# Kernel tuning notes

Measured on AMD Instinct MI355X. Metric: run time of the kernel, lower is better.

Reference implementation:

```python
import jax, jax.numpy as jnp
import numpy as np

NUM = 4
EPS = 1e-8


def setup_inputs() -> dict:
    key = jax.random.key(0)
    ks = jax.random.split(key, 8)
    B, N, D = 64, 1024, 512
    x = jax.random.normal(ks[0], (B, N, D), dtype=jnp.float32)
    # marginal priors: valid probability distributions (log is taken inside)
    p0 = jax.nn.softmax(jax.random.normal(ks[1], (B, 1, D), dtype=jnp.float32), axis=2)
    q0 = jax.nn.softmax(jax.random.normal(ks[2], (B, N, 1), dtype=jnp.float32), axis=1)
    # strictly positive regularization weights / ADMM step sizes
    a1 = jax.random.uniform(ks[3], (NUM,), dtype=jnp.float32, minval=0.1, maxval=1.1)
    a2 = jax.random.uniform(ks[4], (NUM,), dtype=jnp.float32, minval=0.1, maxval=1.1)
    a3 = jax.random.uniform(ks[5], (NUM,), dtype=jnp.float32, minval=0.1, maxval=1.1)
    rho = jax.random.uniform(ks[6], (NUM,), dtype=jnp.float32, minval=0.1, maxval=1.1)
    mask = jnp.ones((B, N, 1), dtype=jnp.float32)
    return {"x": x, "p0": p0, "q0": q0, "a1": a1, "a2": a2, "a3": a3,
            "rho": rho, "mask": mask}


def _lse(y, axis):
    return jax.scipy.special.logsumexp(y, axis=axis, keepdims=True)


def _masked_log_colsum(y, mask):
    # stable log(sum_n exp(y)*mask) over axis 1, masking as in the torch code
    ymin = jnp.min(y, axis=1, keepdims=True)
    ymax = jnp.max(ymin - mask * ymin + y, axis=1, keepdims=True)
    lse = jnp.log(jnp.sum(jnp.exp((y - ymax) * mask) * mask, axis=1, keepdims=True))
    return lse, ymax


def uot_badmm(x, p0, q0, a1, a2, a3, rho, mask, num=NUM, eps=EPS):
    log_p0 = jnp.log(p0)                      # (B,1,D)
    log_q0 = jnp.log(q0 + eps) * mask         # (B,N,1)
    log_t = (log_q0 + log_p0) * mask          # (B,N,D)
    log_s = (log_q0 + log_p0) * mask
    log_mu = jnp.log(p0)
    log_eta = jnp.log(q0 + eps) * mask
    z = jnp.zeros_like(log_t)
    z1 = jnp.zeros_like(p0)
    z2 = jnp.zeros_like(q0)
    for k in range(num):
        n = min(k, a1.shape[0] - 1)
        rn = rho[n]
        # t-update
        y = (x - z) / rn + log_s
        log_t = mask * (log_eta - _lse(y, 2)) + y
        # s-update
        y = (z + rn * log_t) / (a1[n] + rn)
        lse, ymax = _masked_log_colsum(y, mask)
        log_s = mask * (log_mu - lse - ymax) + y
        t = jnp.exp(log_t) * mask
        s = jnp.exp(log_s) * mask
        z = z + rn * (t - s)
        # mu-update
        y = (rn * log_mu + a2[n] * log_p0 - z1) / (rn + a2[n])
        log_mu = y - _lse(y, 2)
        # eta-update
        y = (rn * log_eta + a3[n] * log_q0 - z2) / (rn + a3[n])
        lse, ymax = _masked_log_colsum(y, mask)
        log_eta = (y - lse - ymax) * mask
        # dual updates
        z1 = z1 + rn * (jnp.exp(log_mu) - jnp.sum(s, axis=1, keepdims=True))
        z2 = z2 + rn * (jnp.exp(log_eta) * mask - jnp.sum(t, axis=2, keepdims=True)) * mask
    return jnp.exp(log_t) * mask


def reference(x, p0, q0, a1, a2, a3, rho, mask):
    return uot_badmm(x, p0, q0, a1, a2, a3, rho, mask, num=NUM, eps=EPS)
```

## Files before the change

### kernel.cpp

```cpp
#include <hip/hip_runtime.h>
#include <math.h>

#define BB 64
#define NN 1024
#define DD 512
#define SEG 64
#define ROWS_PER_BLOCK 16
#define ROWS_PER_WAVE 4
#define WAVES 4
#define EPSQ 1e-8f
#define L2E 1.44269504088896340736f

typedef _Float16 h8 __attribute__((ext_vector_type(8)));
typedef float f32x4 __attribute__((ext_vector_type(4)));

#if __has_builtin(__builtin_amdgcn_exp2f)
__device__ __forceinline__ float ex2(float x) { return __builtin_amdgcn_exp2f(x); }
#else
__device__ __forceinline__ float ex2(float x) { return exp2f(x); }
#endif
#if __has_builtin(__builtin_amdgcn_logf)
__device__ __forceinline__ float lg2(float x) { return __builtin_amdgcn_logf(x); }
#else
__device__ __forceinline__ float lg2(float x) { return log2f(x); }
#endif

__device__ __forceinline__ float wmax(float v) {
#pragma unroll
    for (int o = 32; o; o >>= 1) v = fmaxf(v, __shfl_xor(v, o));
    return v;
}
__device__ __forceinline__ float wsum(float v) {
#pragma unroll
    for (int o = 32; o; o >>= 1) v += __shfl_xor(v, o);
    return v;
}
template <int NW>
__device__ __forceinline__ float block_max(float v, float* lds) {
    v = wmax(v);
    __syncthreads();
    if ((threadIdx.x & 63) == 0) lds[threadIdx.x >> 6] = v;
    __syncthreads();
    float r = lds[0];
#pragma unroll
    for (int i = 1; i < NW; i++) r = fmaxf(r, lds[i]);
    return r;
}
template <int NW>
__device__ __forceinline__ float block_sum(float v, float* lds) {
    v = wsum(v);
    __syncthreads();
    if ((threadIdx.x & 63) == 0) lds[threadIdx.x >> 6] = v;
    __syncthreads();
    float r = 0.f;
#pragma unroll
    for (int i = 0; i < NW; i++) r += lds[i];
    return r;
}

__device__ __forceinline__ void load8(float* r, const float* p) {
    float4 a = *reinterpret_cast<const float4*>(p);
    float4 b = *reinterpret_cast<const float4*>(p + 4);
    r[0] = a.x; r[1] = a.y; r[2] = a.z; r[3] = a.w;
    r[4] = b.x; r[5] = b.y; r[6] = b.z; r[7] = b.w;
}
__device__ __forceinline__ void load8_nt(float* r, const float* p) {
    f32x4 a = __builtin_nontemporal_load(reinterpret_cast<const f32x4*>(p));
    f32x4 b = __builtin_nontemporal_load(reinterpret_cast<const f32x4*>(p) + 1);
    r[0] = a.x; r[1] = a.y; r[2] = a.z; r[3] = a.w;
    r[4] = b.x; r[5] = b.y; r[6] = b.z; r[7] = b.w;
}
__device__ __forceinline__ void store8_nt(float* p, const float* r) {
    f32x4 a, b;
    a.x = r[0]; a.y = r[1]; a.z = r[2]; a.w = r[3];
    b.x = r[4]; b.y = r[5]; b.z = r[6]; b.w = r[7];
    __builtin_nontemporal_store(a, reinterpret_cast<f32x4*>(p));
    __builtin_nontemporal_store(b, reinterpret_cast<f32x4*>(p) + 1);
}

__global__ __launch_bounds__(512) void small_seq_kernel(
    const float* __restrict__ p0, const float* __restrict__ q0,
    const float* __restrict__ a2, const float* __restrict__ a3,
    const float* __restrict__ rho, float* __restrict__ lmu_seq,
    float* __restrict__ leta_seq, float* __restrict__ lp_tab) {
    __shared__ float lds[8];
    const int b = blockIdx.x, t = threadIdx.x;
    const float lp = lg2(p0[b * DD + t]);
    lp_tab[b * DD + t] = lp;
    const float lqa = lg2(q0[b * NN + t] + EPSQ);
    const float lqb = lg2(q0[b * NN + t + 512] + EPSQ);
    float lmu = lp, lea = lqa, leb = lqb;
    float z1 = 0.f, z2a = 0.f, z2b = 0.f;
    lmu_seq[b * DD + t] = lmu;
    leta_seq[b * NN + t] = lea;
    leta_seq[b * NN + t + 512] = leb;
    for (int k = 0; k < 4; k++) {
        const float r = rho[k], A2 = a2[k], A3 = a3[k];
        const float rL = r * L2E;
        float y = (r * lmu + A2 * lp - z1) / (r + A2);
        float m = block_max<8>(y, lds);
        float S = block_sum<8>(ex2(y - m), lds);
        float lse = m + lg2(S);
        float lmun = y - lse;
        z1 += rL * (ex2(lmun) - ex2(lmu));
        lmu = lmun;
        if (k < 2) lmu_seq[(size_t)(k + 1) * (BB * DD) + b * DD + t] = lmu;
        float ya = (r * lea + A3 * lqa - z2a) / (r + A3);
        float yb = (r * leb + A3 * lqb - z2b) / (r + A3);
        m = block_max<8>(fmaxf(ya, yb), lds);
        S = block_sum<8>(ex2(ya - m) + ex2(yb - m), lds);
        lse = m + lg2(S);
        float lean = ya - lse, lebn = yb - lse;
        z2a += rL * (ex2(lean) - ex2(lea));
        z2b += rL * (ex2(lebn) - ex2(leb));
        lea = lean;
        leb = lebn;
        if (k < 3) {
            leta_seq[(size_t)(k + 1) * (BB * NN) + b * NN + t] = lea;
            leta_seq[(size_t)(k + 1) * (BB * NN) + b * NN + t + 512] = leb;
        }
    }
}

__global__ __launch_bounds__(256, 4) void a0_kernel(
    const float* __restrict__ x, const float* __restrict__ lp_tab,
    const float* __restrict__ leta_seq, _Float16* __restrict__ x16,
    float* __restrict__ crow, float* __restrict__ psum,
    const float* __restrict__ a1, const float* __restrict__ rho) {
    __shared__ float sms[WAVES][DD];
    const int b = blockIdx.x >> 6, seg = blockIdx.x & 63;
    const int w = threadIdx.x >> 6, l = threadIdx.x & 63;
    const int d0 = l * 8;
    const float r0 = rho[0];
    const float inv_r0 = 1.f / r0;
    const float inv_ar0 = 1.f / (a1[0] + r0);

    float lp[8];
    load8(lp, lp_tab + b * DD + d0);
    const float* lrowq = leta_seq + b * NN;

    float ss[8];
#pragma unroll
    for (int j = 0; j < 8; j++) ss[j] = 0.f;

    const int row0 = seg * ROWS_PER_BLOCK + w * ROWS_PER_WAVE;
#pragma unroll 2
    for (int i = 0; i < ROWS_PER_WAVE; i++) {
        const int n = row0 + i;
        const size_t base = ((size_t)b * NN + n) * DD + d0;
        const float lq = lrowq[n];
        float xv[8];
        load8_nt(xv, x + base);
        h8 xh;
#pragma unroll
        for (int j = 0; j < 8; j++) xh[j] = (_Float16)(xv[j] * L2E);
        *reinterpret_cast<h8*>(x16 + base) = xh;
        float yb[8];
        float ml = -INFINITY;
#pragma unroll
        for (int j = 0; j < 8; j++) {
            float xs = (float)xh[j];
            yb[j] = fmaf(xs, inv_r0, lq + lp[j]);
            ml = fmaxf(ml, yb[j]);
        }
        float m = wmax(ml);
        float se = 0.f;
#pragma unroll
        for (int j = 0; j < 8; j++) se += ex2(yb[j] - m);
        float lse = m + lg2(wsum(se));
        const float c = lq - lse;
        if (l == 0) crow[b * NN + n] = c;
#pragma unroll
        for (int j = 0; j < 8; j++) {
            float lt = c + yb[j];
            ss[j] += ex2((r0 * lt) * inv_ar0);
        }
    }
#pragma unroll
    for (int j = 0; j < 8; j += 4)
        *reinterpret_cast<float4*>(&sms[w][d0 + j]) =
            make_float4(ss[j], ss[j + 1], ss[j + 2], ss[j + 3]);
    __syncthreads();
    for (int d = threadIdx.x; d < DD; d += 256) {
        float S = sms[0][d] + sms[1][d] + sms[2][d] + sms[3][d];
        psum[((size_t)b * SEG + seg) * DD + d] = S;
    }
}

__global__ __launch_bounds__(256) void colfin_kernel(
    const float* __restrict__ psum, const float* __restrict__ lmu_seq,
    float* __restrict__ cc_tab, int k) {
    const int idx = blockIdx.x * 256 + threadIdx.x;
    const int b = idx >> 9, d = idx & (DD - 1);
    float S = 0.f;
    for (int s = 0; s < SEG; s++)
        S += psum[((size_t)b * SEG + s) * DD + d];
    cc_tab[(size_t)k * (BB * DD) + idx] =
        lmu_seq[(size_t)k * (BB * DD) + idx] - lg2(S);
}

template <int K, bool LAST>
__global__ __launch_bounds__(256, 4) void f_kernel(
    const _Float16* __restrict__ x16, float* __restrict__ out,
    const float* __restrict__ lp_tab, const float* __restrict__ leta_seq,
    float* __restrict__ crow, const float* __restrict__ cc_tab,
    float* __restrict__ psum, const float* __restrict__ a1,
    const float* __restrict__ rho) {
    __shared__ float sms[WAVES][DD];
    const int b = blockIdx.x >> 6, seg = blockIdx.x & 63;
    const int w = threadIdx.x >> 6, l = threadIdx.x & 63;
    const int d0 = l * 8;

    float rv[K + 1], invr[K + 1], rLv[K + 1], invar[K + 1];
#pragma unroll
    for (int i = 0; i <= K; i++) {
        rv[i] = rho[i];
        invr[i] = 1.f / rv[i];
        rLv[i] = rv[i] * L2E;
        invar[i] = 1.f / (a1[i] + rv[i]);
    }

    float lp[8];
    load8(lp, lp_tab + b * DD + d0);
    float ccv[K][8];
#pragma unroll
    for (int i = 0; i < K; i++)
        load8(ccv[i], cc_tab + (size_t)i * (BB * DD) + b * DD + d0);

    const float* lrowq = leta_seq + b * NN;
    const float* lrowK = leta_seq + (size_t)K * (BB * NN) + b * NN;

    float ss[8];
#pragma unroll
    for (int j = 0; j < 8; j++) ss[j] = 0.f;

    const int row0 = seg * ROWS_PER_BLOCK + w * ROWS_PER_WAVE;
#pragma unroll 2
    for (int i0 = 0; i0 < ROWS_PER_WAVE; i0++) {
        const int n = row0 + i0;
        const size_t base = ((size_t)b * NN + n) * DD + d0;
        h8 xh;
        if (LAST)
            xh = __builtin_nontemporal_load(
                reinterpret_cast<const h8*>(x16 + base));
        else
            xh = *reinterpret_cast<const h8*>(x16 + base);
        const float lq = lrowq[n];
        float cr[K];
#pragma unroll
        for (int i = 0; i < K; i++) cr[i] = crow[(size_t)i * (BB * NN) + b * NN + n];
        const float letaK = lrowK[n];
        float yb[8], znj[8];
        float ml = -INFINITY;
#pragma unroll
        for (int j = 0; j < 8; j++) {
            float xs = (float)xh[j];
            float y = fmaf(xs, invr[0], lq + lp[j]);
            float lt = cr[0] + y;
            float zn = 0.f;
#pragma unroll
            for (int i = 1; i <= K; i++) {
                float y2v = (zn + rv[i - 1] * lt) * invar[i - 1];
                float ls = ccv[i - 1][j] + y2v;
                zn = zn + rLv[i - 1] * (ex2(lt) - ex2(ls));
                y = fmaf(xs - zn, invr[i], ls);
                if (i < K) lt = cr[i] + y;
            }
            yb[j] = y;
            znj[j] = zn;
            ml = fmaxf(ml, y);
        }
        float m = wmax(ml);
        float se = 0.f;
#pragma unroll
        for (int j = 0; j < 8; j++) se += ex2(yb[j] - m);
        float lse = m + lg2(wsum(se));
        const float c = letaK - lse;
        if (LAST) {
            float o[8];
#pragma unroll
            for (int j = 0; j < 8; j++) o[j] = ex2(c + yb[j]);
            store8_nt(out + base, o);
        } else {
            if (l == 0) crow[(size_t)K * (BB * NN) + b * NN + n] = c;
#pragma unroll
            for (int j = 0; j < 8; j++) {
                float lt = c + yb[j];
                float y2K = (znj[j] + rv[K] * lt) * invar[K];
                ss[j] += ex2(y2K);
            }
        }
    }
    if (!LAST) {
#pragma unroll
        for (int j = 0; j < 8; j += 4)
            *reinterpret_cast<float4*>(&sms[w][d0 + j]) =
                make_float4(ss[j], ss[j + 1], ss[j + 2], ss[j + 3]);
        __syncthreads();
        for (int d = threadIdx.x; d < DD; d += 256) {
            float S = sms[0][d] + sms[1][d] + sms[2][d] + sms[3][d];
            psum[((size_t)b * SEG + seg) * DD + d] = S;
        }
    }
}

extern "C" void kernel_launch(void* const* d_in, const int* in_sizes, int n_in,
                              void* d_out, int out_size, void* d_ws,
                              size_t ws_size, hipStream_t stream) {
    (void)in_sizes; (void)n_in; (void)out_size; (void)ws_size;
    const float* x = (const float*)d_in[0];
    const float* p0 = (const float*)d_in[1];
    const float* q0 = (const float*)d_in[2];
    const float* a1 = (const float*)d_in[3];
    const float* a2 = (const float*)d_in[4];
    const float* a3 = (const float*)d_in[5];
    const float* rho = (const float*)d_in[6];
    float* out = (float*)d_out;

    char* w = (char*)d_ws;
    _Float16* x16 = (_Float16*)w;  w += (size_t)BB * NN * DD * 2;
    float* lmu_seq = (float*)w;    w += (size_t)3 * BB * DD * 4;
    float* leta_seq = (float*)w;   w += (size_t)4 * BB * NN * 4;
    float* psum = (float*)w;       w += (size_t)BB * SEG * DD * 4;
    float* cc_tab = (float*)w;     w += (size_t)3 * BB * DD * 4;
    float* crow = (float*)w;       w += (size_t)3 * BB * NN * 4;
    float* lp_tab = (float*)w;

    const int blocks = BB * SEG;
    const int cfin_blocks = (BB * DD) / 256;

    small_seq_kernel<<<BB, 512, 0, stream>>>(p0, q0, a2, a3, rho, lmu_seq,
                                             leta_seq, lp_tab);
    a0_kernel<<<blocks, 256, 0, stream>>>(x, lp_tab, leta_seq, x16, crow, psum,
                                          a1, rho);

    colfin_kernel<<<cfin_blocks, 256, 0, stream>>>(psum, lmu_seq, cc_tab, 0);
    f_kernel<1, false><<<blocks, 256, 0, stream>>>(
        x16, out, lp_tab, leta_seq, crow, cc_tab, psum, a1, rho);

    colfin_kernel<<<cfin_blocks, 256, 0, stream>>>(psum, lmu_seq, cc_tab, 1);
    f_kernel<2, false><<<blocks, 256, 0, stream>>>(
        x16, out, lp_tab, leta_seq, crow, cc_tab, psum, a1, rho);

    colfin_kernel<<<cfin_blocks, 256, 0, stream>>>(psum, lmu_seq, cc_tab, 2);
    f_kernel<3, true><<<blocks, 256, 0, stream>>>(
        x16, out, lp_tab, leta_seq, crow, cc_tab, psum, a1, rho);
}
```

Measured before the change: 185.8 us.

## Fuse marginal sequence and column finalize into streaming kernels, halve segment count

Folds the small mu/eta sequence kernel into the first streaming kernel, which seg-0 blocks compute, and moves the column-sum finalize into the start of each f_kernel. Every block now redundantly reduces the partial sums into LDS. It also doubles rows per block, halving the number of segments, and recomputes log p0/q0 on the fly instead of reading tables. This cuts four launches and their serialization gaps, at the cost of redundant per-block reductions and a longer seg-0 block.

Result: slower. 190.8 us (+2.7%).

```diff
diff --git a/kernel.cpp b/kernel.cpp
--- a/kernel.cpp
+++ b/kernel.cpp
@@ -4,10 +4,11 @@
 #define BB 64
 #define NN 1024
 #define DD 512
-#define SEG 64
-#define ROWS_PER_BLOCK 16
-#define ROWS_PER_WAVE 4
+#define SEG 32
+#define ROWS_PER_BLOCK 32
+#define ROWS_PER_WAVE 8
 #define WAVES 4
+#define NBLK (BB * SEG)
 #define EPSQ 1e-8f
 #define L2E 1.44269504088896340736f
 
@@ -78,67 +79,85 @@
     __builtin_nontemporal_store(b, reinterpret_cast<f32x4*>(p) + 1);
 }
 
-__global__ __launch_bounds__(512) void small_seq_kernel(
-    const float* __restrict__ p0, const float* __restrict__ q0,
+__global__ __launch_bounds__(256, 4) void k1_kernel(
+    const float* __restrict__ x, const float* __restrict__ p0,
+    const float* __restrict__ q0, const float* __restrict__ a1,
     const float* __restrict__ a2, const float* __restrict__ a3,
-    const float* __restrict__ rho, float* __restrict__ lmu_seq,
-    float* __restrict__ leta_seq, float* __restrict__ lp_tab) {
-    __shared__ float lds[8];
-    const int b = blockIdx.x, t = threadIdx.x;
-    const float lp = lg2(p0[b * DD + t]);
-    lp_tab[b * DD + t] = lp;
-    const float lqa = lg2(q0[b * NN + t] + EPSQ);
-    const float lqb = lg2(q0[b * NN + t + 512] + EPSQ);
-    float lmu = lp, lea = lqa, leb = lqb;
-    float z1 = 0.f, z2a = 0.f, z2b = 0.f;
-    lmu_seq[b * DD + t] = lmu;
-    leta_seq[b * NN + t] = lea;
-    leta_seq[b * NN + t + 512] = leb;
-    for (int k = 0; k < 4; k++) {
-        const float r = rho[k], A2 = a2[k], A3 = a3[k];
-        const float rL = r * L2E;
-        float y = (r * lmu + A2 * lp - z1) / (r + A2);
-        float m = block_max<8>(y, lds);
-        float S = block_sum<8>(ex2(y - m), lds);
-        float lse = m + lg2(S);
-        float lmun = y - lse;
-        z1 += rL * (ex2(lmun) - ex2(lmu));
-        lmu = lmun;
-        if (k < 2) lmu_seq[(size_t)(k + 1) * (BB * DD) + b * DD + t] = lmu;
-        float ya = (r * lea + A3 * lqa - z2a) / (r + A3);
-        float yb = (r * leb + A3 * lqb - z2b) / (r + A3);
-        m = block_max<8>(fmaxf(ya, yb), lds);
-        S = block_sum<8>(ex2(ya - m) + ex2(yb - m), lds);
-        lse = m + lg2(S);
-        float lean = ya - lse, lebn = yb - lse;
-        z2a += rL * (ex2(lean) - ex2(lea));
-        z2b += rL * (ex2(lebn) - ex2(leb));
-        lea = lean;
-        leb = lebn;
-        if (k < 3) {
-            leta_seq[(size_t)(k + 1) * (BB * NN) + b * NN + t] = lea;
-            leta_seq[(size_t)(k + 1) * (BB * NN) + b * NN + t + 512] = leb;
-        }
-    }
-}
-
-__global__ __launch_bounds__(256, 4) void a0_kernel(
-    const float* __restrict__ x, const float* __restrict__ lp_tab,
-    const float* __restrict__ leta_seq, _Float16* __restrict__ x16,
-    float* __restrict__ crow, float* __restrict__ psum,
-    const float* __restrict__ a1, const float* __restrict__ rho) {
+    const float* __restrict__ rho, _Float16* __restrict__ x16,
+    float* __restrict__ lmu_seq, float* __restrict__ leta_seq,
+    float* __restrict__ crow, float* __restrict__ psumA) {
     __shared__ float sms[WAVES][DD];
-    const int b = blockIdx.x >> 6, seg = blockIdx.x & 63;
-    const int w = threadIdx.x >> 6, l = threadIdx.x & 63;
+    __shared__ float s_red[8];
+    const int tid = threadIdx.x;
+    const int b = blockIdx.x >> 5, seg = blockIdx.x & 31;
+    const int w = tid >> 6, l = tid & 63;
     const int d0 = l * 8;
+
+    if (seg == 0) {
+        const float lpA = lg2(p0[b * DD + tid]);
+        const float lpB = lg2(p0[b * DD + tid + 256]);
+        float lqv[4], lev[4], z2v[4];
+#pragma unroll
+        for (int u = 0; u < 4; u++) {
+            lqv[u] = lg2(q0[b * NN + tid + 256 * u] + EPSQ);
+            lev[u] = lqv[u];
+            z2v[u] = 0.f;
+            leta_seq[b * NN + tid + 256 * u] = lqv[u];
+        }
+        float lmuA = lpA, lmuB = lpB, z1A = 0.f, z1B = 0.f;
+        lmu_seq[b * DD + tid] = lmuA;
+        lmu_seq[b * DD + tid + 256] = lmuB;
+        for (int k = 0; k < 3; k++) {
+            const float r = rho[k], A2 = a2[k], A3 = a3[k];
+            const float rL = r * L2E;
+            float yA = (r * lmuA + A2 * lpA - z1A) / (r + A2);
+            float yB = (r * lmuB + A2 * lpB - z1B) / (r + A2);
+            float m = block_max<4>(fmaxf(yA, yB), s_red);
+            float S = block_sum<4>(ex2(yA - m) + ex2(yB - m), s_red);
+            float lse = m + lg2(S);
+            float lmuAn = yA - lse, lmuBn = yB - lse;
+            z1A += rL * (ex2(lmuAn) - ex2(lmuA));
+            z1B += rL * (ex2(lmuBn) - ex2(lmuB));
+            lmuA = lmuAn;
+            lmuB = lmuBn;
+            if (k < 2) {
+                lmu_seq[(size_t)(k + 1) * (BB * DD) + b * DD + tid] = lmuA;
+                lmu_seq[(size_t)(k + 1) * (BB * DD) + b * DD + tid + 256] = lmuB;
+            }
+            float yv[4];
+            float ml = -INFINITY;
+#pragma unroll
+            for (int u = 0; u < 4; u++) {
+                yv[u] = (r * lev[u] + A3 * lqv[u] - z2v[u]) / (r + A3);
+                ml = fmaxf(ml, yv[u]);
+            }
+            m = block_max<4>(ml, s_red);
+            float se = 0.f;
+#pragma unroll
+            for (int u = 0; u < 4; u++) se += ex2(yv[u] - m);
+            S = block_sum<4>(se, s_red);
+            lse = m + lg2(S);
+#pragma unroll
+            for (int u = 0; u < 4; u++) {
+                float ln = yv[u] - lse;
+                z2v[u] += rL * (ex2(ln) - ex2(lev[u]));
+                lev[u] = ln;
+                leta_seq[(size_t)(k + 1) * (BB * NN) + b * NN + tid + 256 * u] = ln;
+            }
+        }
+        __syncthreads();
+    }
+
     const float r0 = rho[0];
     const float inv_r0 = 1.f / r0;
     const float inv_ar0 = 1.f / (a1[0] + r0);
-
     float lp[8];
-    load8(lp, lp_tab + b * DD + d0);
-    const float* lrowq = leta_seq + b * NN;
-
+    {
+        float tmp[8];
+        load8(tmp, p0 + b * DD + d0);
+#pragma unroll
+        for (int j = 0; j < 8; j++) lp[j] = lg2(tmp[j]);
+    }
     float ss[8];
 #pragma unroll
     for (int j = 0; j < 8; j++) ss[j] = 0.f;
@@ -148,7 +167,7 @@
     for (int i = 0; i < ROWS_PER_WAVE; i++) {
         const int n = row0 + i;
         const size_t base = ((size_t)b * NN + n) * DD + d0;
-        const float lq = lrowq[n];
+        const float lq = lg2(q0[b * NN + n] + EPSQ);
         float xv[8];
         load8_nt(xv, x + base);
         h8 xh;
@@ -171,64 +190,70 @@
         const float c = lq - lse;
         if (l == 0) crow[b * NN + n] = c;
 #pragma unroll
-        for (int j = 0; j < 8; j++) {
-            float lt = c + yb[j];
-            ss[j] += ex2((r0 * lt) * inv_ar0);
-        }
+        for (int j = 0; j < 8; j++) ss[j] += ex2((r0 * (c + yb[j])) * inv_ar0);
     }
 #pragma unroll
     for (int j = 0; j < 8; j += 4)
         *reinterpret_cast<float4*>(&sms[w][d0 + j]) =
             make_float4(ss[j], ss[j + 1], ss[j + 2], ss[j + 3]);
     __syncthreads();
-    for (int d = threadIdx.x; d < DD; d += 256) {
+    for (int d = tid; d < DD; d += 256) {
         float S = sms[0][d] + sms[1][d] + sms[2][d] + sms[3][d];
-        psum[((size_t)b * SEG + seg) * DD + d] = S;
-    }
-}
-
-__global__ __launch_bounds__(256) void colfin_kernel(
-    const float* __restrict__ psum, const float* __restrict__ lmu_seq,
-    float* __restrict__ cc_tab, int k) {
-    const int idx = blockIdx.x * 256 + threadIdx.x;
-    const int b = idx >> 9, d = idx & (DD - 1);
-    float S = 0.f;
-    for (int s = 0; s < SEG; s++)
-        S += psum[((size_t)b * SEG + s) * DD + d];
-    cc_tab[(size_t)k * (BB * DD) + idx] =
-        lmu_seq[(size_t)k * (BB * DD) + idx] - lg2(S);
-}
-
-template <int K, bool LAST>
+        psumA[(size_t)blockIdx.x * DD + d] = S;
+    }
+}
+
+template <int P, bool LAST>
 __global__ __launch_bounds__(256, 4) void f_kernel(
     const _Float16* __restrict__ x16, float* __restrict__ out,
-    const float* __restrict__ lp_tab, const float* __restrict__ leta_seq,
-    float* __restrict__ crow, const float* __restrict__ cc_tab,
-    float* __restrict__ psum, const float* __restrict__ a1,
+    const float* __restrict__ p0, const float* __restrict__ lmu_seq,
+    const float* __restrict__ leta_seq, float* __restrict__ crow,
+    float* __restrict__ cc_tab, const float* __restrict__ psum_in,
+    float* __restrict__ psum_out, const float* __restrict__ a1,
     const float* __restrict__ rho) {
+    __shared__ float s_cc[P][DD];
     __shared__ float sms[WAVES][DD];
-    const int b = blockIdx.x >> 6, seg = blockIdx.x & 63;
-    const int w = threadIdx.x >> 6, l = threadIdx.x & 63;
+    const int tid = threadIdx.x;
+    const int b = blockIdx.x >> 5, seg = blockIdx.x & 31;
+    const int w = tid >> 6, l = tid & 63;
     const int d0 = l * 8;
 
-    float rv[K + 1], invr[K + 1], rLv[K + 1], invar[K + 1];
-#pragma unroll
-    for (int i = 0; i <= K; i++) {
+    float rv[P + 1], invr[P + 1], rLv[P + 1], invar[P + 1];
+#pragma unroll
+    for (int i = 0; i <= P; i++) {
         rv[i] = rho[i];
         invr[i] = 1.f / rv[i];
         rLv[i] = rv[i] * L2E;
         invar[i] = 1.f / (a1[i] + rv[i]);
     }
 
+    for (int d = tid; d < DD; d += 256) {
+#pragma unroll
+        for (int i = 0; i + 1 < P; i++)
+            s_cc[i][d] = cc_tab[(size_t)i * (BB * DD) + b * DD + d];
+        float S = 0.f;
+        for (int s = 0; s < SEG; s++)
+            S += psum_in[((size_t)(b * SEG + s)) * DD + d];
+        float ccP = lmu_seq[(size_t)(P - 1) * (BB * DD) + b * DD + d] - lg2(S);
+        s_cc[P - 1][d] = ccP;
+        if (!LAST && seg == 0)
+            cc_tab[(size_t)(P - 1) * (BB * DD) + b * DD + d] = ccP;
+    }
+    __syncthreads();
+
     float lp[8];
-    load8(lp, lp_tab + b * DD + d0);
-    float ccv[K][8];
-#pragma unroll
-    for (int i = 0; i < K; i++)
-        load8(ccv[i], cc_tab + (size_t)i * (BB * DD) + b * DD + d0);
-
-    const float* lrowq = leta_seq + b * NN;
-    const float* lrowK = leta_seq + (size_t)K * (BB * NN) + b * NN;
+    {
+        float tmp[8];
+        load8(tmp, p0 + b * DD + d0);
+#pragma unroll
+        for (int j = 0; j < 8; j++) lp[j] = lg2(tmp[j]);
+    }
+    float ccv[P][8];
+#pragma unroll
+    for (int i = 0; i < P; i++) load8(ccv[i], &s_cc[i][d0]);
+
+    const float* lrow0 = leta_seq + b * NN;
+    const float* lrowP = leta_seq + (size_t)P * (BB * NN) + b * NN;
 
     float ss[8];
 #pragma unroll
@@ -245,50 +270,47 @@
                 reinterpret_cast<const h8*>(x16 + base));
         else
             xh = *reinterpret_cast<const h8*>(x16 + base);
-        const float lq = lrowq[n];
-        float cr[K];
-#pragma unroll
-        for (int i = 0; i < K; i++) cr[i] = crow[(size_t)i * (BB * NN) + b * NN + n];
-        const float letaK = lrowK[n];
-        float yb[8], znj[8];
+        const float lq = lrow0[n];
+        float cr[P];
+#pragma unroll
+        for (int i = 0; i < P; i++)
+            cr[i] = crow[(size_t)i * (BB * NN) + b * NN + n];
+        float y[8], z[8];
         float ml = -INFINITY;
 #pragma unroll
         for (int j = 0; j < 8; j++) {
             float xs = (float)xh[j];
-            float y = fmaf(xs, invr[0], lq + lp[j]);
-            float lt = cr[0] + y;
-            float zn = 0.f;
-#pragma unroll
-            for (int i = 1; i <= K; i++) {
-                float y2v = (zn + rv[i - 1] * lt) * invar[i - 1];
-                float ls = ccv[i - 1][j] + y2v;
-                zn = zn + rLv[i - 1] * (ex2(lt) - ex2(ls));
-                y = fmaf(xs - zn, invr[i], ls);
-                if (i < K) lt = cr[i] + y;
+            float yy = fmaf(xs, invr[0], lq + lp[j]);
+            float lt = cr[0] + yy;
+            float zz = 0.f;
+#pragma unroll
+            for (int i2 = 1; i2 <= P; i2++) {
+                float y2v = (zz + rv[i2 - 1] * lt) * invar[i2 - 1];
+                float ls = ccv[i2 - 1][j] + y2v;
+                zz += rLv[i2 - 1] * (ex2(lt) - ex2(ls));
+                yy = fmaf(xs - zz, invr[i2], ls);
+                if (i2 < P) lt = cr[i2] + yy;
             }
-            yb[j] = y;
-            znj[j] = zn;
-            ml = fmaxf(ml, y);
+            y[j] = yy;
+            z[j] = zz;
+            ml = fmaxf(ml, yy);
         }
         float m = wmax(ml);
         float se = 0.f;
 #pragma unroll
-        for (int j = 0; j < 8; j++) se += ex2(yb[j] - m);
+        for (int j = 0; j < 8; j++) se += ex2(y[j] - m);
         float lse = m + lg2(wsum(se));
-        const float c = letaK - lse;
+        const float c = lrowP[n] - lse;
         if (LAST) {
             float o[8];
 #pragma unroll
-            for (int j = 0; j < 8; j++) o[j] = ex2(c + yb[j]);
+            for (int j = 0; j < 8; j++) o[j] = ex2(c + y[j]);
             store8_nt(out + base, o);
         } else {
-            if (l == 0) crow[(size_t)K * (BB * NN) + b * NN + n] = c;
-#pragma unroll
-            for (int j = 0; j < 8; j++) {
-                float lt = c + yb[j];
-                float y2K = (znj[j] + rv[K] * lt) * invar[K];
-                ss[j] += ex2(y2K);
-            }
+            if (l == 0) crow[(size_t)P * (BB * NN) + b * NN + n] = c;
+#pragma unroll
+            for (int j = 0; j < 8; j++)
+                ss[j] += ex2((z[j] + rv[P] * (c + y[j])) * invar[P]);
         }
     }
     if (!LAST) {
@@ -297,9 +319,9 @@
             *reinterpret_cast<float4*>(&sms[w][d0 + j]) =
                 make_float4(ss[j], ss[j + 1], ss[j + 2], ss[j + 3]);
         __syncthreads();
-        for (int d = threadIdx.x; d < DD; d += 256) {
+        for (int d = tid; d < DD; d += 256) {
             float S = sms[0][d] + sms[1][d] + sms[2][d] + sms[3][d];
-            psum[((size_t)b * SEG + seg) * DD + d] = S;
+            psum_out[(size_t)blockIdx.x * DD + d] = S;
         }
     }
 }
@@ -321,28 +343,17 @@
     _Float16* x16 = (_Float16*)w;  w += (size_t)BB * NN * DD * 2;
     float* lmu_seq = (float*)w;    w += (size_t)3 * BB * DD * 4;
     float* leta_seq = (float*)w;   w += (size_t)4 * BB * NN * 4;
-    float* psum = (float*)w;       w += (size_t)BB * SEG * DD * 4;
-    float* cc_tab = (float*)w;     w += (size_t)3 * BB * DD * 4;
-    float* crow = (float*)w;       w += (size_t)3 * BB * NN * 4;
-    float* lp_tab = (float*)w;
-
-    const int blocks = BB * SEG;
-    const int cfin_blocks = (BB * DD) / 256;
-
-    small_seq_kernel<<<BB, 512, 0, stream>>>(p0, q0, a2, a3, rho, lmu_seq,
-                                             leta_seq, lp_tab);
-    a0_kernel<<<blocks, 256, 0, stream>>>(x, lp_tab, leta_seq, x16, crow, psum,
-                                          a1, rho);
-
-    colfin_kernel<<<cfin_blocks, 256, 0, stream>>>(psum, lmu_seq, cc_tab, 0);
-    f_kernel<1, false><<<blocks, 256, 0, stream>>>(
-        x16, out, lp_tab, leta_seq, crow, cc_tab, psum, a1, rho);
-
-    colfin_kernel<<<cfin_blocks, 256, 0, stream>>>(psum, lmu_seq, cc_tab, 1);
-    f_kernel<2, false><<<blocks, 256, 0, stream>>>(
-        x16, out, lp_tab, leta_seq, crow, cc_tab, psum, a1, rho);
-
-    colfin_kernel<<<cfin_blocks, 256, 0, stream>>>(psum, lmu_seq, cc_tab, 2);
-    f_kernel<3, true><<<blocks, 256, 0, stream>>>(
-        x16, out, lp_tab, leta_seq, crow, cc_tab, psum, a1, rho);
-}
+    float* psumA = (float*)w;      w += (size_t)NBLK * DD * 4;
+    float* psumB = (float*)w;      w += (size_t)NBLK * DD * 4;
+    float* cc_tab = (float*)w;     w += (size_t)2 * BB * DD * 4;
+    float* crow = (float*)w;
+
+    k1_kernel<<<NBLK, 256, 0, stream>>>(x, p0, q0, a1, a2, a3, rho, x16,
+                                        lmu_seq, leta_seq, crow, psumA);
+    f_kernel<1, false><<<NBLK, 256, 0, stream>>>(
+        x16, out, p0, lmu_seq, leta_seq, crow, cc_tab, psumA, psumB, a1, rho);
+    f_kernel<2, false><<<NBLK, 256, 0, stream>>>(
+        x16, out, p0, lmu_seq, leta_seq, crow, cc_tab, psumB, psumA, a1, rho);
+    f_kernel<3, true><<<NBLK, 256, 0, stream>>>(
+        x16, out, p0, lmu_seq, leta_seq, crow, cc_tab, psumA, psumB, a1, rho);
+}
```

## Switch to single-wave blocks with per-wave column partial sums

Applied to the files above, without the earlier changes.

Blocks shrink from four waves to one wave of 64 threads covering 4 rows, which removes the LDS reduction and __syncthreads in the main kernels. Each block writes its own column partial sums, so the colfin reduction now reads 256 segments instead of 64. log2 of p0 and q0 is recomputed inside the kernels instead of being read from a precomputed table. Launch bounds differ per template stage, and psum uses ping-pong buffers. The cost is four times more partial-sum traffic and a longer serial loop in colfin.

New measurement: 249.8 us. 34.5% more time.

```diff
diff --git a/kernel.cpp b/kernel.cpp
--- a/kernel.cpp
+++ b/kernel.cpp
@@ -4,10 +4,9 @@
 #define BB 64
 #define NN 1024
 #define DD 512
-#define SEG 64
-#define ROWS_PER_BLOCK 16
-#define ROWS_PER_WAVE 4
-#define WAVES 4
+#define RPW 4
+#define SEGB (NN / RPW)
+#define NBLK (BB * SEGB)
 #define EPSQ 1e-8f
 #define L2E 1.44269504088896340736f
 
@@ -77,16 +76,22 @@
     __builtin_nontemporal_store(a, reinterpret_cast<f32x4*>(p));
     __builtin_nontemporal_store(b, reinterpret_cast<f32x4*>(p) + 1);
 }
+__device__ __forceinline__ void store8(float* p, const float* r) {
+    float4 a, b;
+    a.x = r[0]; a.y = r[1]; a.z = r[2]; a.w = r[3];
+    b.x = r[4]; b.y = r[5]; b.z = r[6]; b.w = r[7];
+    *reinterpret_cast<float4*>(p) = a;
+    *reinterpret_cast<float4*>(p + 4) = b;
+}
 
 __global__ __launch_bounds__(512) void small_seq_kernel(
     const float* __restrict__ p0, const float* __restrict__ q0,
     const float* __restrict__ a2, const float* __restrict__ a3,
     const float* __restrict__ rho, float* __restrict__ lmu_seq,
-    float* __restrict__ leta_seq, float* __restrict__ lp_tab) {
+    float* __restrict__ leta_seq) {
     __shared__ float lds[8];
     const int b = blockIdx.x, t = threadIdx.x;
     const float lp = lg2(p0[b * DD + t]);
-    lp_tab[b * DD + t] = lp;
     const float lqa = lg2(q0[b * NN + t] + EPSQ);
     const float lqb = lg2(q0[b * NN + t + 512] + EPSQ);
     float lmu = lp, lea = lqa, leb = lqb;
@@ -94,7 +99,7 @@
     lmu_seq[b * DD + t] = lmu;
     leta_seq[b * NN + t] = lea;
     leta_seq[b * NN + t + 512] = leb;
-    for (int k = 0; k < 4; k++) {
+    for (int k = 0; k < 3; k++) {
         const float r = rho[k], A2 = a2[k], A3 = a3[k];
         const float rL = r * L2E;
         float y = (r * lmu + A2 * lp - z1) / (r + A2);
@@ -115,40 +120,41 @@
         z2b += rL * (ex2(lebn) - ex2(leb));
         lea = lean;
         leb = lebn;
-        if (k < 3) {
-            leta_seq[(size_t)(k + 1) * (BB * NN) + b * NN + t] = lea;
-            leta_seq[(size_t)(k + 1) * (BB * NN) + b * NN + t + 512] = leb;
-        }
-    }
-}
-
-__global__ __launch_bounds__(256, 4) void a0_kernel(
-    const float* __restrict__ x, const float* __restrict__ lp_tab,
-    const float* __restrict__ leta_seq, _Float16* __restrict__ x16,
-    float* __restrict__ crow, float* __restrict__ psum,
+        leta_seq[(size_t)(k + 1) * (BB * NN) + b * NN + t] = lea;
+        leta_seq[(size_t)(k + 1) * (BB * NN) + b * NN + t + 512] = leb;
+    }
+}
+
+__global__ __launch_bounds__(64, 8) void a0_kernel(
+    const float* __restrict__ x, const float* __restrict__ p0,
+    const float* __restrict__ q0, _Float16* __restrict__ x16,
+    float* __restrict__ crow, float* __restrict__ psumA,
     const float* __restrict__ a1, const float* __restrict__ rho) {
-    __shared__ float sms[WAVES][DD];
-    const int b = blockIdx.x >> 6, seg = blockIdx.x & 63;
-    const int w = threadIdx.x >> 6, l = threadIdx.x & 63;
+    const int blk = blockIdx.x;
+    const int b = blk >> 8, seg = blk & 255;
+    const int l = threadIdx.x;
     const int d0 = l * 8;
     const float r0 = rho[0];
     const float inv_r0 = 1.f / r0;
     const float inv_ar0 = 1.f / (a1[0] + r0);
 
     float lp[8];
-    load8(lp, lp_tab + b * DD + d0);
-    const float* lrowq = leta_seq + b * NN;
-
+    {
+        float tmp[8];
+        load8(tmp, p0 + b * DD + d0);
+#pragma unroll
+        for (int j = 0; j < 8; j++) lp[j] = lg2(tmp[j]);
+    }
     float ss[8];
 #pragma unroll
     for (int j = 0; j < 8; j++) ss[j] = 0.f;
 
-    const int row0 = seg * ROWS_PER_BLOCK + w * ROWS_PER_WAVE;
+    const int row0 = seg * RPW;
 #pragma unroll 2
-    for (int i = 0; i < ROWS_PER_WAVE; i++) {
+    for (int i = 0; i < RPW; i++) {
         const int n = row0 + i;
         const size_t base = ((size_t)b * NN + n) * DD + d0;
-        const float lq = lrowq[n];
+        const float lq = lg2(q0[b * NN + n] + EPSQ);
         float xv[8];
         load8_nt(xv, x + base);
         h8 xh;
@@ -171,20 +177,9 @@
         const float c = lq - lse;
         if (l == 0) crow[b * NN + n] = c;
 #pragma unroll
-        for (int j = 0; j < 8; j++) {
-            float lt = c + yb[j];
-            ss[j] += ex2((r0 * lt) * inv_ar0);
-        }
-    }
-#pragma unroll
-    for (int j = 0; j < 8; j += 4)
-        *reinterpret_cast<float4*>(&sms[w][d0 + j]) =
-            make_float4(ss[j], ss[j + 1], ss[j + 2], ss[j + 3]);
-    __syncthreads();
-    for (int d = threadIdx.x; d < DD; d += 256) {
-        float S = sms[0][d] + sms[1][d] + sms[2][d] + sms[3][d];
-        psum[((size_t)b * SEG + seg) * DD + d] = S;
-    }
+        for (int j = 0; j < 8; j++) ss[j] += ex2((r0 * (c + yb[j])) * inv_ar0);
+    }
+    store8(psumA + (size_t)blk * DD + d0, ss);
 }
 
 __global__ __launch_bounds__(256) void colfin_kernel(
@@ -193,27 +188,27 @@
     const int idx = blockIdx.x * 256 + threadIdx.x;
     const int b = idx >> 9, d = idx & (DD - 1);
     float S = 0.f;
-    for (int s = 0; s < SEG; s++)
-        S += psum[((size_t)b * SEG + s) * DD + d];
+    for (int s = 0; s < SEGB; s++)
+        S += psum[((size_t)(b * SEGB + s)) * DD + d];
     cc_tab[(size_t)k * (BB * DD) + idx] =
         lmu_seq[(size_t)k * (BB * DD) + idx] - lg2(S);
 }
 
-template <int K, bool LAST>
-__global__ __launch_bounds__(256, 4) void f_kernel(
+template <int P, bool LAST, int MINW>
+__global__ __launch_bounds__(64, MINW) void f_kernel(
     const _Float16* __restrict__ x16, float* __restrict__ out,
-    const float* __restrict__ lp_tab, const float* __restrict__ leta_seq,
+    const float* __restrict__ p0, const float* __restrict__ leta_seq,
     float* __restrict__ crow, const float* __restrict__ cc_tab,
-    float* __restrict__ psum, const float* __restrict__ a1,
+    float* __restrict__ psum_out, const float* __restrict__ a1,
     const float* __restrict__ rho) {
-    __shared__ float sms[WAVES][DD];
-    const int b = blockIdx.x >> 6, seg = blockIdx.x & 63;
-    const int w = threadIdx.x >> 6, l = threadIdx.x & 63;
+    const int blk = blockIdx.x;
+    const int b = blk >> 8, seg = blk & 255;
+    const int l = threadIdx.x;
     const int d0 = l * 8;
 
-    float rv[K + 1], invr[K + 1], rLv[K + 1], invar[K + 1];
-#pragma unroll
-    for (int i = 0; i <= K; i++) {
+    float rv[P + 1], invr[P + 1], rLv[P + 1], invar[P + 1];
+#pragma unroll
+    for (int i = 0; i <= P; i++) {
         rv[i] = rho[i];
         invr[i] = 1.f / rv[i];
         rLv[i] = rv[i] * L2E;
@@ -221,22 +216,27 @@
     }
 
     float lp[8];
-    load8(lp, lp_tab + b * DD + d0);
-    float ccv[K][8];
-#pragma unroll
-    for (int i = 0; i < K; i++)
+    {
+        float tmp[8];
+        load8(tmp, p0 + b * DD + d0);
+#pragma unroll
+        for (int j = 0; j < 8; j++) lp[j] = lg2(tmp[j]);
+    }
+    float ccv[P][8];
+#pragma unroll
+    for (int i = 0; i < P; i++)
         load8(ccv[i], cc_tab + (size_t)i * (BB * DD) + b * DD + d0);
 
-    const float* lrowq = leta_seq + b * NN;
-    const float* lrowK = leta_seq + (size_t)K * (BB * NN) + b * NN;
+    const float* lrow0 = leta_seq + b * NN;
+    const float* lrowP = leta_seq + (size_t)P * (BB * NN) + b * NN;
 
     float ss[8];
 #pragma unroll
     for (int j = 0; j < 8; j++) ss[j] = 0.f;
 
-    const int row0 = seg * ROWS_PER_BLOCK + w * ROWS_PER_WAVE;
+    const int row0 = seg * RPW;
 #pragma unroll 2
-    for (int i0 = 0; i0 < ROWS_PER_WAVE; i0++) {
+    for (int i0 = 0; i0 < RPW; i0++) {
         const int n = row0 + i0;
         const size_t base = ((size_t)b * NN + n) * DD + d0;
         h8 xh;
@@ -245,63 +245,50 @@
                 reinterpret_cast<const h8*>(x16 + base));
         else
             xh = *reinterpret_cast<const h8*>(x16 + base);
-        const float lq = lrowq[n];
-        float cr[K];
-#pragma unroll
-        for (int i = 0; i < K; i++) cr[i] = crow[(size_t)i * (BB * NN) + b * NN + n];
-        const float letaK = lrowK[n];
-        float yb[8], znj[8];
+        const float lq = lrow0[n];
+        float cr[P];
+#pragma unroll
+        for (int i = 0; i < P; i++)
+            cr[i] = crow[(size_t)i * (BB * NN) + b * NN + n];
+        float y[8], z[8];
         float ml = -INFINITY;
 #pragma unroll
         for (int j = 0; j < 8; j++) {
             float xs = (float)xh[j];
-            float y = fmaf(xs, invr[0], lq + lp[j]);
-            float lt = cr[0] + y;
-            float zn = 0.f;
-#pragma unroll
-            for (int i = 1; i <= K; i++) {
-                float y2v = (zn + rv[i - 1] * lt) * invar[i - 1];
-                float ls = ccv[i - 1][j] + y2v;
-                zn = zn + rLv[i - 1] * (ex2(lt) - ex2(ls));
-                y = fmaf(xs - zn, invr[i], ls);
-                if (i < K) lt = cr[i] + y;
+            float yy = fmaf(xs, invr[0], lq + lp[j]);
+            float lt = cr[0] + yy;
+            float zz = 0.f;
+#pragma unroll
+            for (int i2 = 1; i2 <= P; i2++) {
+                float y2v = (zz + rv[i2 - 1] * lt) * invar[i2 - 1];
+                float ls = ccv[i2 - 1][j] + y2v;
+                zz += rLv[i2 - 1] * (ex2(lt) - ex2(ls));
+                yy = fmaf(xs - zz, invr[i2], ls);
+                if (i2 < P) lt = cr[i2] + yy;
             }
-            yb[j] = y;
-            znj[j] = zn;
-            ml = fmaxf(ml, y);
+            y[j] = yy;
+            z[j] = zz;
+            ml = fmaxf(ml, yy);
         }
         float m = wmax(ml);
         float se = 0.f;
 #pragma unroll
-        for (int j = 0; j < 8; j++) se += ex2(yb[j] - m);
+        for (int j = 0; j < 8; j++) se += ex2(y[j] - m);
         float lse = m + lg2(wsum(se));
-        const float c = letaK - lse;
+        const float c = lrowP[n] - lse;
         if (LAST) {
             float o[8];
 #pragma unroll
-            for (int j = 0; j < 8; j++) o[j] = ex2(c + yb[j]);
+            for (int j = 0; j < 8; j++) o[j] = ex2(c + y[j]);
             store8_nt(out + base, o);
         } else {
-            if (l == 0) crow[(size_t)K * (BB * NN) + b * NN + n] = c;
-#pragma unroll
-            for (int j = 0; j < 8; j++) {
-                float lt = c + yb[j];
-                float y2K = (znj[j] + rv[K] * lt) * invar[K];
-                ss[j] += ex2(y2K);
-            }
+            if (l == 0) crow[(size_t)P * (BB * NN) + b * NN + n] = c;
+#pragma unroll
+            for (int j = 0; j < 8; j++)
+                ss[j] += ex2((z[j] + rv[P] * (c + y[j])) * invar[P]);
         }
     }
-    if (!LAST) {
-#pragma unroll
-        for (int j = 0; j < 8; j += 4)
-            *reinterpret_cast<float4*>(&sms[w][d0 + j]) =
-                make_float4(ss[j], ss[j + 1], ss[j + 2], ss[j + 3]);
-        __syncthreads();
-        for (int d = threadIdx.x; d < DD; d += 256) {
-            float S = sms[0][d] + sms[1][d] + sms[2][d] + sms[3][d];
-            psum[((size_t)b * SEG + seg) * DD + d] = S;
-        }
-    }
+    if (!LAST) store8(psum_out + (size_t)blk * DD + d0, ss);
 }
 
 extern "C" void kernel_launch(void* const* d_in, const int* in_sizes, int n_in,
@@ -321,28 +308,26 @@
     _Float16* x16 = (_Float16*)w;  w += (size_t)BB * NN * DD * 2;
     float* lmu_seq = (float*)w;    w += (size_t)3 * BB * DD * 4;
     float* leta_seq = (float*)w;   w += (size_t)4 * BB * NN * 4;
-    float* psum = (float*)w;       w += (size_t)BB * SEG * DD * 4;
+    float* psumA = (float*)w;      w += (size_t)NBLK * DD * 4;
+    float* psumB = (float*)w;      w += (size_t)NBLK * DD * 4;
     float* cc_tab = (float*)w;     w += (size_t)3 * BB * DD * 4;
-    float* crow = (float*)w;       w += (size_t)3 * BB * NN * 4;
-    float* lp_tab = (float*)w;
-
-    const int blocks = BB * SEG;
+    float* crow = (float*)w;
+
     const int cfin_blocks = (BB * DD) / 256;
 
     small_seq_kernel<<<BB, 512, 0, stream>>>(p0, q0, a2, a3, rho, lmu_seq,
-                                             leta_seq, lp_tab);
-    a0_kernel<<<blocks, 256, 0, stream>>>(x, lp_tab, leta_seq, x16, crow, psum,
-                                          a1, rho);
-
-    colfin_kernel<<<cfin_blocks, 256, 0, stream>>>(psum, lmu_seq, cc_tab, 0);
-    f_kernel<1, false><<<blocks, 256, 0, stream>>>(
-        x16, out, lp_tab, leta_seq, crow, cc_tab, psum, a1, rho);
-
-    colfin_kernel<<<cfin_blocks, 256, 0, stream>>>(psum, lmu_seq, cc_tab, 1);
-    f_kernel<2, false><<<blocks, 256, 0, stream>>>(
-        x16, out, lp_tab, leta_seq, crow, cc_tab, psum, a1, rho);
-
-    colfin_kernel<<<cfin_blocks, 256, 0, stream>>>(psum, lmu_seq, cc_tab, 2);
-    f_kernel<3, true><<<blocks, 256, 0, stream>>>(
-        x16, out, lp_tab, leta_seq, crow, cc_tab, psum, a1, rho);
-}
+                                             leta_seq);
+    a0_kernel<<<NBLK, 64, 0, stream>>>(x, p0, q0, x16, crow, psumA, a1, rho);
+
+    colfin_kernel<<<cfin_blocks, 256, 0, stream>>>(psumA, lmu_seq, cc_tab, 0);
+    f_kernel<1, false, 8><<<NBLK, 64, 0, stream>>>(
+        x16, out, p0, leta_seq, crow, cc_tab, psumB, a1, rho);
+
+    colfin_kernel<<<cfin_blocks, 256, 0, stream>>>(psumB, lmu_seq, cc_tab, 1);
+    f_kernel<2, false, 7><<<NBLK, 64, 0, stream>>>(
+        x16, out, p0, leta_seq, crow, cc_tab, psumA, a1, rho);
+
+    colfin_kernel<<<cfin_blocks, 256, 0, stream>>>(psumA, lmu_seq, cc_tab, 2);
+    f_kernel<3, true, 6><<<NBLK, 64, 0, stream>>>(
+        x16, out, p0, leta_seq, crow, cc_tab, psumB, a1, rho);
+}
```
